# Optimization experiments

Hardware: AMD Instinct MI355X
Metric: run time of the kernel (lower is better)

## Reference

```python
import jax, jax.numpy as jnp
import numpy as np

IN_FEATURES = 16384
OUT_FEATURES = 16384
NNZ = 1_000_000
BATCH = 256


def setup_inputs() -> dict:
    key = jax.random.key(0)
    k_x, k_w, k_b, k_r, k_c = jax.random.split(key, 5)
    x = jax.random.normal(k_x, (BATCH, IN_FEATURES), dtype=jnp.float32)
    weight_vals = jax.random.normal(k_w, (NNZ,), dtype=jnp.float32)
    bias = jax.random.normal(k_b, (OUT_FEATURES,), dtype=jnp.float32)
    rows = jax.random.randint(k_r, (NNZ,), 0, OUT_FEATURES, dtype=jnp.int32)
    cols = jax.random.randint(k_c, (NNZ,), 0, IN_FEATURES, dtype=jnp.int32)
    return {"x": x, "weight_vals": weight_vals, "bias": bias,
            "rows": rows, "cols": cols}


def reference(x, weight_vals, bias, rows, cols):
    # SparseLinear forward: y = x @ W^T + b, with W sparse COO of shape
    # [out_features, in_features]; (rows, cols) are W's nnz coordinates.
    # Per-edge contribution: x[:, col] * W[row, col], scattered into out[:, row].
    contrib = x[:, cols] * weight_vals  # [B, nnz]
    # segment-sum edges into output features: [nnz, B] -> [out, B]
    out = jax.ops.segment_sum(contrib.T, rows, num_segments=OUT_FEATURES).T
    return out + bias  # [B, out_features]
```

## Files before the change

### kernel.cpp

```cpp
#include <hip/hip_runtime.h>
#include <hip/hip_bf16.h>
#include <hip/hip_fp16.h>

#define BATCH_N 256
#define IN_F    16384
#define OUT_F   16384
#define CAP     128
#define NBUCK   512
#define CAPB    2560
#define EPB     2048
#define TBLK    1024

typedef unsigned int u32x4 __attribute__((ext_vector_type(4)));
typedef float f32x4 __attribute__((ext_vector_type(4)));


__global__ void prep_kernel(const float* __restrict__ x,
                            __hip_bfloat16* __restrict__ xTh,
                            const int* __restrict__ rows,
                            const int* __restrict__ cols,
                            const float* __restrict__ vals, int nnz,
                            int* __restrict__ gcursor,
                            uint2* __restrict__ staging) {
    __shared__ int smem[64 * 65];
    int t = threadIdx.x;
    if (blockIdx.x < TBLK) {
        float* tile = (float*)smem;
        int bid = blockIdx.x;
        int i0 = (bid & 255) * 64;
        int b0 = (bid >> 8) * 64;
        int tx4 = t & 15;
        int r16 = t >> 4;
#pragma unroll
        for (int k = 0; k < 4; ++k) {
            int row = r16 + k * 16;
            f32x4 v = *(const f32x4*)(x + (size_t)(b0 + row) * IN_F + i0 + tx4 * 4);
            tile[row * 65 + tx4 * 4 + 0] = v.x;
            tile[row * 65 + tx4 * 4 + 1] = v.y;
            tile[row * 65 + tx4 * 4 + 2] = v.z;
            tile[row * 65 + tx4 * 4 + 3] = v.w;
        }
        __syncthreads();
        int tx = t & 63, ty = t >> 6;
        int h = b0 >> 7, j0 = b0 & 127;
#pragma unroll
        for (int k = 0; k < 64; k += 4) {
            int col = i0 + ty + k;
            xTh[((size_t)h * IN_F + col) * 128 + j0 + tx] =
                __float2bfloat16(tile[tx * 65 + ty + k]);
        }
    } else {
        int* hist = smem;
        int* base = smem + NBUCK;
        hist[t] = 0; hist[t + 256] = 0;
        __syncthreads();
        int i0 = (blockIdx.x - TBLK) * EPB;
        unsigned int pack[8], vb[8];
        int bk[8];
#pragma unroll
        for (int k = 0; k < 8; ++k) {
            int i = i0 + k * 256 + t;
            if (i < nnz) {
                int r = rows[i], c = cols[i];
                pack[k] = ((unsigned int)r << 14) | (unsigned int)c;
                vb[k] = __float_as_uint(vals[i]);
                bk[k] = r >> 5;
                atomicAdd(&hist[bk[k]], 1);
            } else bk[k] = -1;
        }
        __syncthreads();
#pragma unroll
        for (int q = 0; q < 2; ++q) {
            int bin = t + q * 256;
            int h = hist[bin];
            base[bin] = (h > 0) ? atomicAdd(&gcursor[bin], h) : 0;
        }
        __syncthreads();
        hist[t] = 0; hist[t + 256] = 0;
        __syncthreads();
#pragma unroll
        for (int k = 0; k < 8; ++k) {
            if (bk[k] >= 0) {
                int p = base[bk[k]] + atomicAdd(&hist[bk[k]], 1);
                if (p < CAPB)
                    staging[(size_t)bk[k] * CAPB + p] = make_uint2(pack[k], vb[k]);
            }
        }
    }
}


__global__ void __launch_bounds__(512)
bucket_scatter_kernel(const uint2* __restrict__ staging,
                      const int* __restrict__ gcursor,
                      unsigned int* __restrict__ edges,
                      int* __restrict__ counts) {
    __shared__ int lcnt[32];
    __shared__ unsigned int lbin[32 * CAP];
    int b = blockIdx.x;
    int t = threadIdx.x;
    if (t < 32) lcnt[t] = 0;
    __syncthreads();
    int n = gcursor[b];
    if (n > CAPB) n = CAPB;
    const uint2* st = staging + (size_t)b * CAPB;
    for (int i = t; i < n; i += 512) {
        uint2 rec = __builtin_nontemporal_load((const unsigned long long*)st + i)
                        ? make_uint2(0, 0) : make_uint2(0, 0);
        (void)rec;
        uint2 r2;
        {
            unsigned long long v =
                __builtin_nontemporal_load((const unsigned long long*)st + i);
            r2.x = (unsigned int)(v & 0xffffffffull);
            r2.y = (unsigned int)(v >> 32);
        }
        int rl = (r2.x >> 14) & 31;
        int p = atomicAdd(&lcnt[rl], 1);
        if (p < CAP) {
            unsigned int col = r2.x & 16383u;
            __half hv = __float2half(__uint_as_float(r2.y));
            lbin[rl * CAP + p] = (col << 16) | (unsigned int)__half_as_ushort(hv);
        }
    }
    __syncthreads();
    if (t < 32) {
        int c = lcnt[t];
        if (c > CAP) c = CAP;
        counts[b * 32 + t] = (c + 7) & ~7;
    }
    unsigned int* dst = edges + (size_t)b * 32 * CAP;
    for (int i4 = t; i4 < 32 * CAP / 4; i4 += 512) {
        int i = i4 * 4;
        int row = i >> 7;
        int slot = i & (CAP - 1);
        int c = lcnt[row];
        if (c > CAP) c = CAP;
        int lim = (c + 7) & ~7;
        if (slot < lim) {
            u32x4 v;
            v.x = (slot + 0 < c) ? lbin[i + 0] : 0u;
            v.y = (slot + 1 < c) ? lbin[i + 1] : 0u;
            v.z = (slot + 2 < c) ? lbin[i + 2] : 0u;
            v.w = (slot + 3 < c) ? lbin[i + 3] : 0u;
            __builtin_nontemporal_store(v, (u32x4*)(dst + i));
        }
    }
}


__global__ void accum_kernel(const unsigned int* __restrict__ xh0,
                             const unsigned int* __restrict__ edges,
                             const int*   __restrict__ counts,
                             const float* __restrict__ bias,
                             float* __restrict__ out) {
    __shared__ float slab[128][17];
    int blk = blockIdx.x;
    int h = blk & 1;
    int o0 = (blk >> 1) * 16;
    int w = threadIdx.x >> 6;
    int lane = threadIdx.x & 63;
    const unsigned int* xh = xh0 + (size_t)h * IN_F * 64;
#pragma unroll
    for (int rr = 0; rr < 4; ++rr) {
        int rl = w * 4 + rr;
        int o = __builtin_amdgcn_readfirstlane(o0 + rl);
        int n = counts[o];
        const u32x4* el4 = (const u32x4*)(edges + (size_t)o * CAP);
        float ax = 0.f, ay = 0.f;
        u32x4 ca = el4[0], cb = el4[1];
        for (int j = 0; j < n; j += 8) {
            u32x4 na = el4[(j >> 2) + 2];
            u32x4 nb = el4[(j >> 2) + 3];
            unsigned int e[8];
            e[0] = ca.x; e[1] = ca.y; e[2] = ca.z; e[3] = ca.w;
            e[4] = cb.x; e[5] = cb.y; e[6] = cb.z; e[7] = cb.w;
            unsigned int g[8];
#pragma unroll
            for (int k = 0; k < 8; ++k) {
                const unsigned int* p = xh + ((e[k] >> 16) << 6);
                g[k] = p[lane];
            }
#pragma unroll
            for (int k = 0; k < 8; ++k) {
                float v = __half2float(__ushort_as_half((unsigned short)(e[k] & 0xffffu)));
                ax += __uint_as_float(g[k] << 16) * v;
                ay += __uint_as_float(g[k] & 0xffff0000u) * v;
            }
            ca = na; cb = nb;
        }
        float bv = bias[o];
        slab[2 * lane + 0][rl] = ax + bv;
        slab[2 * lane + 1][rl] = ay + bv;
    }
    __syncthreads();
#pragma unroll
    for (int it = 0; it < 2; ++it) {
        int item = threadIdx.x + it * 256;
        int bl = item >> 2;
        int q = item & 3;
        f32x4 v;
        v.x = slab[bl][q * 4 + 0];
        v.y = slab[bl][q * 4 + 1];
        v.z = slab[bl][q * 4 + 2];
        v.w = slab[bl][q * 4 + 3];
        __builtin_nontemporal_store(v,
            (f32x4*)(out + (size_t)(h * 128 + bl) * OUT_F + o0 + q * 4));
    }
}

extern "C" void kernel_launch(void* const* d_in, const int* in_sizes, int n_in,
                              void* d_out, int out_size, void* d_ws, size_t ws_size,
                              hipStream_t stream) {
    const float* x     = (const float*)d_in[0];
    const float* wvals = (const float*)d_in[1];
    const float* bias  = (const float*)d_in[2];
    const int*   rows  = (const int*)d_in[3];
    const int*   cols  = (const int*)d_in[4];
    float* out = (float*)d_out;
    int nnz = in_sizes[1];

    const size_t MB = 1024 * 1024;
    char* ws = (char*)d_ws;
    __hip_bfloat16* xTh = (__hip_bfloat16*)(ws);
    uint2* staging = (uint2*)(ws + 8 * MB);
    unsigned int* edges = (unsigned int*)(ws + 22 * MB);
    int*   gcursor = (int*)(ws + 30 * MB);
    int*   counts  = (int*)(ws + 30 * MB + 4096);

    (void)hipMemsetAsync(gcursor, 0, NBUCK * sizeof(int), stream);

    int npart = (nnz + EPB - 1) / EPB;
    prep_kernel<<<TBLK + npart, 256, 0, stream>>>(x, xTh, rows, cols, wvals, nnz,
                                                  gcursor, staging);
    bucket_scatter_kernel<<<NBUCK, 512, 0, stream>>>(staging, gcursor, edges, counts);
    accum_kernel<<<(OUT_F / 16) * 2, 256, 0, stream>>>((const unsigned int*)xTh, edges,
                                                       counts, bias, out);
}
```

Measured before the change: 140.0 us.

## Scatter edges directly into per-row slots with global atomics, drop bucket pass

Replaces the two-stage bucket sort (block-local histogram into staging buffer, then a separate bucket_scatter kernel) with direct per-edge global atomicAdd on per-row counters, writing each packed edge straight into its row slot. The edges buffer and counters are zeroed by a single larger memset so padding slots read as zero, and the accum kernel now clamps and rounds the count itself. This removes one kernel launch and the staging round trip, but adds about a million contended global atomics, scattered 4-byte writes, and an 8 MB memset. Edge-block work is also ordered before the transpose blocks in the grid.

```diff
diff --git a/kernel.cpp b/kernel.cpp
--- a/kernel.cpp
+++ b/kernel.cpp
@@ -6,8 +6,6 @@
 #define IN_F    16384
 #define OUT_F   16384
 #define CAP     128
-#define NBUCK   512
-#define CAPB    2560
 #define EPB     2048
 #define TBLK    1024
 
@@ -19,14 +17,27 @@
                             __hip_bfloat16* __restrict__ xTh,
                             const int* __restrict__ rows,
                             const int* __restrict__ cols,
-                            const float* __restrict__ vals, int nnz,
-                            int* __restrict__ gcursor,
-                            uint2* __restrict__ staging) {
-    __shared__ int smem[64 * 65];
+                            const float* __restrict__ vals, int nnz, int npart,
+                            unsigned int* __restrict__ edges,
+                            int* __restrict__ counts) {
+    __shared__ float tile[64 * 65];
     int t = threadIdx.x;
-    if (blockIdx.x < TBLK) {
-        float* tile = (float*)smem;
-        int bid = blockIdx.x;
+    if ((int)blockIdx.x < npart) {
+        int i0 = blockIdx.x * EPB;
+#pragma unroll
+        for (int k = 0; k < 8; ++k) {
+            int i = i0 + k * 256 + t;
+            if (i < nnz) {
+                int r = rows[i];
+                unsigned int rec = ((unsigned int)cols[i] << 16) |
+                    (unsigned int)__half_as_ushort(__float2half(vals[i]));
+                int p = atomicAdd(&counts[r], 1);
+                if (p < CAP)
+                    edges[(size_t)r * CAP + p] = rec;
+            }
+        }
+    } else {
+        int bid = blockIdx.x - npart;
         int i0 = (bid & 255) * 64;
         int b0 = (bid >> 8) * 64;
         int tx4 = t & 15;
@@ -49,102 +60,6 @@
             xTh[((size_t)h * IN_F + col) * 128 + j0 + tx] =
                 __float2bfloat16(tile[tx * 65 + ty + k]);
         }
-    } else {
-        int* hist = smem;
-        int* base = smem + NBUCK;
-        hist[t] = 0; hist[t + 256] = 0;
-        __syncthreads();
-        int i0 = (blockIdx.x - TBLK) * EPB;
-        unsigned int pack[8], vb[8];
-        int bk[8];
-#pragma unroll
-        for (int k = 0; k < 8; ++k) {
-            int i = i0 + k * 256 + t;
-            if (i < nnz) {
-                int r = rows[i], c = cols[i];
-                pack[k] = ((unsigned int)r << 14) | (unsigned int)c;
-                vb[k] = __float_as_uint(vals[i]);
-                bk[k] = r >> 5;
-                atomicAdd(&hist[bk[k]], 1);
-            } else bk[k] = -1;
-        }
-        __syncthreads();
-#pragma unroll
-        for (int q = 0; q < 2; ++q) {
-            int bin = t + q * 256;
-            int h = hist[bin];
-            base[bin] = (h > 0) ? atomicAdd(&gcursor[bin], h) : 0;
-        }
-        __syncthreads();
-        hist[t] = 0; hist[t + 256] = 0;
-        __syncthreads();
-#pragma unroll
-        for (int k = 0; k < 8; ++k) {
-            if (bk[k] >= 0) {
-                int p = base[bk[k]] + atomicAdd(&hist[bk[k]], 1);
-                if (p < CAPB)
-                    staging[(size_t)bk[k] * CAPB + p] = make_uint2(pack[k], vb[k]);
-            }
-        }
-    }
-}
-
-
-__global__ void __launch_bounds__(512)
-bucket_scatter_kernel(const uint2* __restrict__ staging,
-                      const int* __restrict__ gcursor,
-                      unsigned int* __restrict__ edges,
-                      int* __restrict__ counts) {
-    __shared__ int lcnt[32];
-    __shared__ unsigned int lbin[32 * CAP];
-    int b = blockIdx.x;
-    int t = threadIdx.x;
-    if (t < 32) lcnt[t] = 0;
-    __syncthreads();
-    int n = gcursor[b];
-    if (n > CAPB) n = CAPB;
-    const uint2* st = staging + (size_t)b * CAPB;
-    for (int i = t; i < n; i += 512) {
-        uint2 rec = __builtin_nontemporal_load((const unsigned long long*)st + i)
-                        ? make_uint2(0, 0) : make_uint2(0, 0);
-        (void)rec;
-        uint2 r2;
-        {
-            unsigned long long v =
-                __builtin_nontemporal_load((const unsigned long long*)st + i);
-            r2.x = (unsigned int)(v & 0xffffffffull);
-            r2.y = (unsigned int)(v >> 32);
-        }
-        int rl = (r2.x >> 14) & 31;
-        int p = atomicAdd(&lcnt[rl], 1);
-        if (p < CAP) {
-            unsigned int col = r2.x & 16383u;
-            __half hv = __float2half(__uint_as_float(r2.y));
-            lbin[rl * CAP + p] = (col << 16) | (unsigned int)__half_as_ushort(hv);
-        }
-    }
-    __syncthreads();
-    if (t < 32) {
-        int c = lcnt[t];
-        if (c > CAP) c = CAP;
-        counts[b * 32 + t] = (c + 7) & ~7;
-    }
-    unsigned int* dst = edges + (size_t)b * 32 * CAP;
-    for (int i4 = t; i4 < 32 * CAP / 4; i4 += 512) {
-        int i = i4 * 4;
-        int row = i >> 7;
-        int slot = i & (CAP - 1);
-        int c = lcnt[row];
-        if (c > CAP) c = CAP;
-        int lim = (c + 7) & ~7;
-        if (slot < lim) {
-            u32x4 v;
-            v.x = (slot + 0 < c) ? lbin[i + 0] : 0u;
-            v.y = (slot + 1 < c) ? lbin[i + 1] : 0u;
-            v.z = (slot + 2 < c) ? lbin[i + 2] : 0u;
-            v.w = (slot + 3 < c) ? lbin[i + 3] : 0u;
-            __builtin_nontemporal_store(v, (u32x4*)(dst + i));
-        }
     }
 }
 
@@ -165,7 +80,9 @@
     for (int rr = 0; rr < 4; ++rr) {
         int rl = w * 4 + rr;
         int o = __builtin_amdgcn_readfirstlane(o0 + rl);
-        int n = counts[o];
+        int cnt = counts[o];
+        if (cnt > CAP) cnt = CAP;
+        int n = (cnt + 7) & ~7;
         const u32x4* el4 = (const u32x4*)(edges + (size_t)o * CAP);
         float ax = 0.f, ay = 0.f;
         u32x4 ca = el4[0], cb = el4[1];
@@ -223,17 +140,14 @@
     const size_t MB = 1024 * 1024;
     char* ws = (char*)d_ws;
     __hip_bfloat16* xTh = (__hip_bfloat16*)(ws);
-    uint2* staging = (uint2*)(ws + 8 * MB);
-    unsigned int* edges = (unsigned int*)(ws + 22 * MB);
-    int*   gcursor = (int*)(ws + 30 * MB);
-    int*   counts  = (int*)(ws + 30 * MB + 4096);
+    unsigned int* edges = (unsigned int*)(ws + 8 * MB);
+    int* counts = (int*)(ws + 16 * MB);
 
-    (void)hipMemsetAsync(gcursor, 0, NBUCK * sizeof(int), stream);
+    (void)hipMemsetAsync(ws + 8 * MB, 0, 8 * MB + OUT_F * sizeof(int), stream);
 
     int npart = (nnz + EPB - 1) / EPB;
-    prep_kernel<<<TBLK + npart, 256, 0, stream>>>(x, xTh, rows, cols, wvals, nnz,
-                                                  gcursor, staging);
-    bucket_scatter_kernel<<<NBUCK, 512, 0, stream>>>(staging, gcursor, edges, counts);
+    prep_kernel<<<npart + TBLK, 256, 0, stream>>>(x, xTh, rows, cols, wvals, nnz,
+                                                  npart, edges, counts);
     accum_kernel<<<(OUT_F / 16) * 2, 256, 0, stream>>>((const unsigned int*)xTh, edges,
                                                        counts, bias, out);
 }
```

New measurement: 168.8 us. +20.6%, slower.

## Fuse bucket scatter into accumulation kernel, binning edges in shared memory

Applied to the files above, without the earlier changes.

Removes the separate bucket_scatter kernel and its global edges/counts buffers. Each accum block now reads its bucket's staging records directly, bins them per output row in LDS, and then gathers from the transposed bf16 x. The packed col|half value is built in prep. Each wave processes two rows at once with scalar edge indices taken by readfirstlane, and bias is added at the final store. Each of the two batch-half blocks redoes the LDS binning for the same bucket, and there are fewer blocks with 32 rows each, which may hurt load balance.

```diff
diff --git a/kernel.cpp b/kernel.cpp
--- a/kernel.cpp
+++ b/kernel.cpp
@@ -2,7 +2,6 @@
 #include <hip/hip_bf16.h>
 #include <hip/hip_fp16.h>
 
-#define BATCH_N 256
 #define IN_F    16384
 #define OUT_F   16384
 #define CAP     128
@@ -63,7 +62,9 @@
             if (i < nnz) {
                 int r = rows[i], c = cols[i];
                 pack[k] = ((unsigned int)r << 14) | (unsigned int)c;
-                vb[k] = __float_as_uint(vals[i]);
+                __half hv = __float2half(vals[i]);
+                vb[k] = ((unsigned int)c << 16) |
+                        (unsigned int)__half_as_ushort(hv);
                 bk[k] = r >> 5;
                 atomicAdd(&hist[bk[k]], 1);
             } else bk[k] = -1;
@@ -90,120 +91,105 @@
 }
 
 
-__global__ void __launch_bounds__(512)
-bucket_scatter_kernel(const uint2* __restrict__ staging,
-                      const int* __restrict__ gcursor,
-                      unsigned int* __restrict__ edges,
-                      int* __restrict__ counts) {
+__global__ void __launch_bounds__(512, 4)
+accum_kernel(const unsigned int* __restrict__ xh0,
+             const uint2* __restrict__ staging,
+             const int* __restrict__ gcursor,
+             const float* __restrict__ bias,
+             float* __restrict__ out) {
+    __shared__ union {
+        unsigned int lbin[32 * CAP];
+        float slab[32 * 129];
+    } u;
     __shared__ int lcnt[32];
-    __shared__ unsigned int lbin[32 * CAP];
-    int b = blockIdx.x;
+    int blk = blockIdx.x;
+    int h = blk & 1;
+    int bu = blk >> 1;
+    int o0 = bu * 32;
     int t = threadIdx.x;
+    int w = t >> 6, lane = t & 63;
+    {
+        u32x4 z = {0u, 0u, 0u, 0u};
+#pragma unroll
+        for (int i = 0; i < 2; ++i)
+            *(u32x4*)&u.lbin[(t + i * 512) * 4] = z;
+    }
     if (t < 32) lcnt[t] = 0;
     __syncthreads();
-    int n = gcursor[b];
+    int n = gcursor[bu];
     if (n > CAPB) n = CAPB;
-    const uint2* st = staging + (size_t)b * CAPB;
+    const uint2* st = staging + (size_t)bu * CAPB;
     for (int i = t; i < n; i += 512) {
-        uint2 rec = __builtin_nontemporal_load((const unsigned long long*)st + i)
-                        ? make_uint2(0, 0) : make_uint2(0, 0);
-        (void)rec;
-        uint2 r2;
-        {
-            unsigned long long v =
-                __builtin_nontemporal_load((const unsigned long long*)st + i);
-            r2.x = (unsigned int)(v & 0xffffffffull);
-            r2.y = (unsigned int)(v >> 32);
-        }
+        uint2 r2 = st[i];
         int rl = (r2.x >> 14) & 31;
         int p = atomicAdd(&lcnt[rl], 1);
-        if (p < CAP) {
-            unsigned int col = r2.x & 16383u;
-            __half hv = __float2half(__uint_as_float(r2.y));
-            lbin[rl * CAP + p] = (col << 16) | (unsigned int)__half_as_ushort(hv);
-        }
-    }
-    __syncthreads();
-    if (t < 32) {
-        int c = lcnt[t];
-        if (c > CAP) c = CAP;
-        counts[b * 32 + t] = (c + 7) & ~7;
-    }
-    unsigned int* dst = edges + (size_t)b * 32 * CAP;
-    for (int i4 = t; i4 < 32 * CAP / 4; i4 += 512) {
-        int i = i4 * 4;
-        int row = i >> 7;
-        int slot = i & (CAP - 1);
-        int c = lcnt[row];
-        if (c > CAP) c = CAP;
-        int lim = (c + 7) & ~7;
-        if (slot < lim) {
-            u32x4 v;
-            v.x = (slot + 0 < c) ? lbin[i + 0] : 0u;
-            v.y = (slot + 1 < c) ? lbin[i + 1] : 0u;
-            v.z = (slot + 2 < c) ? lbin[i + 2] : 0u;
-            v.w = (slot + 3 < c) ? lbin[i + 3] : 0u;
-            __builtin_nontemporal_store(v, (u32x4*)(dst + i));
-        }
-    }
-}
-
-
-__global__ void accum_kernel(const unsigned int* __restrict__ xh0,
-                             const unsigned int* __restrict__ edges,
-                             const int*   __restrict__ counts,
-                             const float* __restrict__ bias,
-                             float* __restrict__ out) {
-    __shared__ float slab[128][17];
-    int blk = blockIdx.x;
-    int h = blk & 1;
-    int o0 = (blk >> 1) * 16;
-    int w = threadIdx.x >> 6;
-    int lane = threadIdx.x & 63;
+        if (p < CAP) u.lbin[rl * CAP + p] = r2.y;
+    }
+    __syncthreads();
     const unsigned int* xh = xh0 + (size_t)h * IN_F * 64;
+    float aa[4], ab[4];
+#pragma unroll
+    for (int pp = 0; pp < 2; ++pp) {
+        int rlA = w * 4 + pp * 2;
+        int rlB = rlA + 1;
+        int cA = lcnt[rlA]; if (cA > CAP) cA = CAP;
+        int cB = lcnt[rlB]; if (cB > CAP) cB = CAP;
+        int cm = cA > cB ? cA : cB;
+        int lim = (cm + 3) & ~3;
+        const u32x4* lbA = (const u32x4*)&u.lbin[rlA * CAP];
+        const u32x4* lbB = (const u32x4*)&u.lbin[rlB * CAP];
+        float a0 = 0.f, a1 = 0.f, b0 = 0.f, b1 = 0.f;
+        if (lim > 0) {
+            u32x4 curA = lbA[0], curB = lbB[0];
+            for (int j = 0; j < lim; j += 4) {
+                u32x4 nxtA = lbA[(j >> 2) + 1];
+                u32x4 nxtB = lbB[(j >> 2) + 1];
+                unsigned int eA[4] = {curA.x, curA.y, curA.z, curA.w};
+                unsigned int eB[4] = {curB.x, curB.y, curB.z, curB.w};
+                unsigned int sA[4], sB[4], gA[4], gB[4];
+#pragma unroll
+                for (int k = 0; k < 4; ++k) {
+                    sA[k] = __builtin_amdgcn_readfirstlane(eA[k]);
+                    sB[k] = __builtin_amdgcn_readfirstlane(eB[k]);
+                    gA[k] = *(xh + ((sA[k] >> 16) << 6) + lane);
+                    gB[k] = *(xh + ((sB[k] >> 16) << 6) + lane);
+                }
+#pragma unroll
+                for (int k = 0; k < 4; ++k) {
+                    float vA = __half2float(__ushort_as_half(
+                                   (unsigned short)(sA[k] & 0xffffu)));
+                    float vB = __half2float(__ushort_as_half(
+                                   (unsigned short)(sB[k] & 0xffffu)));
+                    a0 += __uint_as_float(gA[k] << 16) * vA;
+                    a1 += __uint_as_float(gA[k] & 0xffff0000u) * vA;
+                    b0 += __uint_as_float(gB[k] << 16) * vB;
+                    b1 += __uint_as_float(gB[k] & 0xffff0000u) * vB;
+                }
+                curA = nxtA; curB = nxtB;
+            }
+        }
+        aa[pp * 2 + 0] = a0; ab[pp * 2 + 0] = a1;
+        aa[pp * 2 + 1] = b0; ab[pp * 2 + 1] = b1;
+    }
+    __syncthreads();
 #pragma unroll
     for (int rr = 0; rr < 4; ++rr) {
         int rl = w * 4 + rr;
-        int o = __builtin_amdgcn_readfirstlane(o0 + rl);
-        int n = counts[o];
-        const u32x4* el4 = (const u32x4*)(edges + (size_t)o * CAP);
-        float ax = 0.f, ay = 0.f;
-        u32x4 ca = el4[0], cb = el4[1];
-        for (int j = 0; j < n; j += 8) {
-            u32x4 na = el4[(j >> 2) + 2];
-            u32x4 nb = el4[(j >> 2) + 3];
-            unsigned int e[8];
-            e[0] = ca.x; e[1] = ca.y; e[2] = ca.z; e[3] = ca.w;
-            e[4] = cb.x; e[5] = cb.y; e[6] = cb.z; e[7] = cb.w;
-            unsigned int g[8];
-#pragma unroll
-            for (int k = 0; k < 8; ++k) {
-                const unsigned int* p = xh + ((e[k] >> 16) << 6);
-                g[k] = p[lane];
-            }
-#pragma unroll
-            for (int k = 0; k < 8; ++k) {
-                float v = __half2float(__ushort_as_half((unsigned short)(e[k] & 0xffffu)));
-                ax += __uint_as_float(g[k] << 16) * v;
-                ay += __uint_as_float(g[k] & 0xffff0000u) * v;
-            }
-            ca = na; cb = nb;
-        }
-        float bv = bias[o];
-        slab[2 * lane + 0][rl] = ax + bv;
-        slab[2 * lane + 1][rl] = ay + bv;
+        u.slab[rl * 129 + 2 * lane + 0] = aa[rr];
+        u.slab[rl * 129 + 2 * lane + 1] = ab[rr];
     }
     __syncthreads();
 #pragma unroll
     for (int it = 0; it < 2; ++it) {
-        int item = threadIdx.x + it * 256;
-        int bl = item >> 2;
-        int q = item & 3;
+        int item = t + it * 512;
+        int bl = item >> 3;
+        int q = item & 7;
+        f32x4 bv = *(const f32x4*)(bias + o0 + q * 4);
         f32x4 v;
-        v.x = slab[bl][q * 4 + 0];
-        v.y = slab[bl][q * 4 + 1];
-        v.z = slab[bl][q * 4 + 2];
-        v.w = slab[bl][q * 4 + 3];
+        v.x = u.slab[(q * 4 + 0) * 129 + bl] + bv.x;
+        v.y = u.slab[(q * 4 + 1) * 129 + bl] + bv.y;
+        v.z = u.slab[(q * 4 + 2) * 129 + bl] + bv.z;
+        v.w = u.slab[(q * 4 + 3) * 129 + bl] + bv.w;
         __builtin_nontemporal_store(v,
             (f32x4*)(out + (size_t)(h * 128 + bl) * OUT_F + o0 + q * 4));
     }
@@ -224,16 +210,13 @@
     char* ws = (char*)d_ws;
     __hip_bfloat16* xTh = (__hip_bfloat16*)(ws);
     uint2* staging = (uint2*)(ws + 8 * MB);
-    unsigned int* edges = (unsigned int*)(ws + 22 * MB);
-    int*   gcursor = (int*)(ws + 30 * MB);
-    int*   counts  = (int*)(ws + 30 * MB + 4096);
+    int*   gcursor = (int*)(ws + 20 * MB);
 
     (void)hipMemsetAsync(gcursor, 0, NBUCK * sizeof(int), stream);
 
     int npart = (nnz + EPB - 1) / EPB;
     prep_kernel<<<TBLK + npart, 256, 0, stream>>>(x, xTh, rows, cols, wvals, nnz,
                                                   gcursor, staging);
-    bucket_scatter_kernel<<<NBUCK, 512, 0, stream>>>(staging, gcursor, edges, counts);
-    accum_kernel<<<(OUT_F / 16) * 2, 256, 0, stream>>>((const unsigned int*)xTh, edges,
-                                                       counts, bias, out);
+    accum_kernel<<<NBUCK * 2, 512, 0, stream>>>((const unsigned int*)xTh, staging,
+                                                gcursor, bias, out);
 }
```

Measured after the change: 134.0 us. -4.2%, faster.
